# Optimization experiments

Hardware: AMD Instinct MI355X
Metric: run time of the kernel (lower is better)

Reference implementation:

```python
import jax, jax.numpy as jnp
import numpy as np

N_POINTS = 1048576  # batch of evaluation points
HIDDEN = 128
N_HIDDEN_LAYERS = 9  # 128->128 layers between the input and output projections


def setup_inputs() -> dict:
    key = jax.random.key(0)
    ks = jax.random.split(key, 7)
    # Kaiming-ish scale so activations stay O(1) through the deep ReLU stack
    s_in = (2.0 / 4) ** 0.5
    s_h = (2.0 / HIDDEN) ** 0.5
    return {
        "x": jax.random.normal(ks[0], (N_POINTS, 4), dtype=jnp.float32),
        "W0": jax.random.normal(ks[1], (HIDDEN, 4), dtype=jnp.float32) * s_in,
        "b0": jnp.zeros((HIDDEN,), dtype=jnp.float32),
        "Wh": jax.random.normal(ks[2], (N_HIDDEN_LAYERS, HIDDEN, HIDDEN), dtype=jnp.float32) * s_h,
        "bh": jnp.zeros((N_HIDDEN_LAYERS, HIDDEN), dtype=jnp.float32),
        "Wout": jax.random.normal(ks[3], (1, HIDDEN), dtype=jnp.float32) * s_h,
        "bout": jnp.zeros((1,), dtype=jnp.float32),
    }


def reference(x, W0, b0, Wh, bh, Wout, bout):
    # Flatten: x is already [N, 4]; nn.Flatten collapses trailing dims to 4.
    h = jax.nn.relu(jnp.einsum("nd,hd->nh", x, W0) + b0)  # [N, 128]
    # 9 hidden Linear(128,128)+ReLU layers; small fixed layer loop (structural)
    for i in range(N_HIDDEN_LAYERS):
        h = jax.nn.relu(jnp.einsum("nh,oh->no", h, Wh[i]) + bh[i])
    logits = jnp.einsum("nh,oh->no", h, Wout) + bout  # [N, 1], no final ReLU
    return logits
```

## Files before the change

kernel.cpp:

```cpp
#include <hip/hip_runtime.h>
#include <stdint.h>

typedef _Float16 f16x8 __attribute__((ext_vector_type(8)));
typedef __fp16   fp16x2 __attribute__((ext_vector_type(2)));
typedef float    f32x16 __attribute__((ext_vector_type(16)));

union Frag {
  f16x8    v;
  uint32_t w[4];
  _Float16 h[8];
};

union CVec {
  float4 q[4];
  f32x16 v;
};

__device__ __forceinline__ uint32_t pack2h(float a, float b) {
  union { _Float16 h[2]; uint32_t u; } r;
  r.h[0] = (_Float16)a;
  r.h[1] = (_Float16)b;
  return r.u;
}

__device__ __forceinline__ uint32_t pkrtz(float a, float b) {
  union { fp16x2 h2; uint32_t u; } cv;
  cv.h2 = __builtin_amdgcn_cvt_pkrtz(a, b);
  return cv.u;
}

__device__ __forceinline__ void g2lds16(const void* g, void* l) {
  __builtin_amdgcn_global_load_lds(
      (const __attribute__((address_space(1))) uint32_t*)g,
      (__attribute__((address_space(3))) uint32_t*)l, 16, 0, 0);
}

__host__ __device__ __forceinline__ int lam32(int s) {
  return (((s >> 2) ^ (s >> 3)) & 1) ? (s ^ 12) : s;
}

__global__ void prep_kernel(const float* __restrict__ W0, const float* __restrict__ b0,
                            const float* __restrict__ Wh, const float* __restrict__ bh,
                            const float* __restrict__ Wout,
                            _Float16* __restrict__ wfrag, _Float16* __restrict__ w0frag,
                            float* __restrict__ biasC, _Float16* __restrict__ woutf16) {
  const int stride = gridDim.x * blockDim.x;
  for (int idx = blockIdx.x * blockDim.x + threadIdx.x; idx < 154880; idx += stride) {
    if (idx < 147456) {
      const int j = idx & 7, lane = (idx >> 3) & 63, kt = (idx >> 9) & 7,
                ot = (idx >> 12) & 3, l = idx >> 14;
      const int o = ot * 32 + lam32(lane & 31);
      const int k = kt * 16 + (lane >> 5) * 8 + j;
      wfrag[idx] = (_Float16)Wh[(l * 128 + o) * 128 + k];
    } else if (idx < 147456 + 2048) {
      const int i = idx - 147456;
      const int j = i & 7, lane = (i >> 3) & 63, ot = i >> 9;
      const int o = ot * 32 + lam32(lane & 31);
      const int k = (lane >> 5) * 8 + j;
      w0frag[i] = (_Float16)(k < 4 ? W0[o * 4 + k] : 0.0f);
    } else if (idx < 147456 + 2048 + 1280) {
      const int i = idx - (147456 + 2048);
      const int r = i & 15, hh = (i >> 4) & 1, ot = (i >> 5) & 3, l = i >> 7;
      const int slot = (r & 3) + 8 * (r >> 2) + 4 * hh;
      const int o = ot * 32 + lam32(slot);
      biasC[i] = (l == 0) ? b0[o] : bh[(l - 1) * 128 + o];
    } else {
      const int i = idx - (147456 + 2048 + 1280);
      const int j = i & 7, lane = (i >> 3) & 63, kt = i >> 9;
      const int k = kt * 16 + (lane >> 5) * 8 + j;
      woutf16[i] = ((lane & 31) == 0) ? (_Float16)Wout[k] : (_Float16)0.0f;
    }
  }
}

__global__ __launch_bounds__(256, 2) void mlp_fused(
    const float* __restrict__ x,
    const _Float16* __restrict__ wfrag,
    const _Float16* __restrict__ w0frag,
    const float* __restrict__ biasCg,
    const _Float16* __restrict__ woutf16,
    const float* __restrict__ boutp,
    float* __restrict__ out) {
  __shared__ __align__(16) unsigned char ldsW[2][32768];
  __shared__ __align__(16) float ldsBiasC[1280];

  const int t    = threadIdx.x;
  const int lane = t & 63;
  const int wv   = t >> 6;
  const int h    = lane >> 5;
  const int ln   = lane & 31;
  const long rowbase = (long)blockIdx.x * 256 + wv * 64;

  {
    const unsigned char* src = (const unsigned char*)wfrag;
#pragma unroll
    for (int i = 0; i < 8; ++i) {
      const int off = i * 4096 + t * 16;
      g2lds16(src + off, &ldsW[0][off]);
    }
    const unsigned char* bsrc = (const unsigned char*)biasCg;
    g2lds16(bsrc + t * 16, (unsigned char*)ldsBiasC + t * 16);
    if (t < 64) g2lds16(bsrc + (256 + t) * 16, (unsigned char*)ldsBiasC + (256 + t) * 16);
  }

  Frag   B[2][8];
  f32x16 acc[4][2];
  const f32x16 fzero = (f32x16)0.0f;

  auto load_cvec = [&](int l, int ot) -> f32x16 {
    CVec cv;
    const float* p = ldsBiasC + ((l * 4 + ot) * 2 + h) * 16;
#pragma unroll
    for (int g = 0; g < 4; ++g) cv.q[g] = *(const float4*)(p + g * 4);
    return cv.v;
  };

  Frag xb[2];
#pragma unroll
  for (int nt = 0; nt < 2; ++nt) {
    float4 xv = make_float4(0.f, 0.f, 0.f, 0.f);
    if (h == 0) xv = *(const float4*)(x + (rowbase + nt * 32 + ln) * 4);
    xb[nt].w[0] = pack2h(xv.x, xv.y);
    xb[nt].w[1] = pack2h(xv.z, xv.w);
    xb[nt].w[2] = 0u;
    xb[nt].w[3] = 0u;
  }

  __syncthreads();

#pragma unroll
  for (int ot = 0; ot < 4; ++ot) {
    const f16x8 a0 = *(const f16x8*)(w0frag + ot * 512 + lane * 8);
    const f32x16 cvec = load_cvec(0, ot);
    acc[ot][0] = __builtin_amdgcn_mfma_f32_32x32x16_f16(a0, xb[0].v, cvec, 0, 0, 0);
    acc[ot][1] = __builtin_amdgcn_mfma_f32_32x32x16_f16(a0, xb[1].v, cvec, 0, 0, 0);
  }

  auto do_epilogue = [&]() {
#pragma unroll
    for (int ot = 0; ot < 4; ++ot) {
#pragma unroll
      for (int nt = 0; nt < 2; ++nt) {
#pragma unroll
        for (int u = 0; u < 2; ++u) {
          Frag nb;
#pragma unroll
          for (int j = 0; j < 4; ++j) {
            const uint32_t cv = pkrtz(acc[ot][nt][8 * u + 2 * j],
                                      acc[ot][nt][8 * u + 2 * j + 1]);
            uint32_t r;
            asm("v_pk_max_f16 %0, %1, %2" : "=v"(r) : "v"(cv), "v"(0u));
            nb.w[j] = r;
          }
          B[nt][ot * 2 + u] = nb;
        }
      }
    }
  };

#pragma unroll
  for (int l = 1; l <= 9; ++l) {
    if (l < 9) {
      const unsigned char* src = (const unsigned char*)wfrag + (size_t)l * 32768;
#pragma unroll
      for (int i = 0; i < 8; ++i) {
        const int off = i * 4096 + t * 16;
        g2lds16(src + off, &ldsW[l & 1][off]);
      }
    }
    do_epilogue();
    const unsigned char* wl = &ldsW[(l - 1) & 1][0];

    f16x8 a[4];
#pragma unroll
    for (int ot = 0; ot < 4; ++ot)
      a[ot] = *(const f16x8*)(wl + ot * 8192 + lane * 16);

#pragma unroll
    for (int kt = 0; kt < 8; ++kt) {
#pragma unroll
      for (int ot = 0; ot < 4; ++ot) {
        if (kt == 0) {
          const f32x16 cvec = load_cvec(l, ot);
          acc[ot][0] = __builtin_amdgcn_mfma_f32_32x32x16_f16(a[ot], B[0][kt].v, cvec, 0, 0, 0);
          acc[ot][1] = __builtin_amdgcn_mfma_f32_32x32x16_f16(a[ot], B[1][kt].v, cvec, 0, 0, 0);
        } else {
          acc[ot][0] = __builtin_amdgcn_mfma_f32_32x32x16_f16(a[ot], B[0][kt].v, acc[ot][0], 0, 0, 0);
          acc[ot][1] = __builtin_amdgcn_mfma_f32_32x32x16_f16(a[ot], B[1][kt].v, acc[ot][1], 0, 0, 0);
        }
        if (kt < 7)
          a[ot] = *(const f16x8*)(wl + ot * 8192 + (kt + 1) * 1024 + lane * 16);
        __builtin_amdgcn_sched_group_barrier(0x008, 2, 0);
        if (kt < 7)
          __builtin_amdgcn_sched_group_barrier(0x100, 1, 0);
      }
    }
    if (l < 9) __syncthreads();
  }

  {
    Frag wa[8];
#pragma unroll
    for (int kt = 0; kt < 8; ++kt)
      wa[kt].v = *(const f16x8*)(woutf16 + kt * 512 + lane * 8);
    const float boutv = *boutp;

    do_epilogue();

    f32x16 accO0 = fzero, accO1 = fzero;
#pragma unroll
    for (int kt = 0; kt < 8; ++kt) {
      accO0 = __builtin_amdgcn_mfma_f32_32x32x16_f16(wa[kt].v, B[0][kt].v, accO0, 0, 0, 0);
      accO1 = __builtin_amdgcn_mfma_f32_32x32x16_f16(wa[kt].v, B[1][kt].v, accO1, 0, 0, 0);
    }
    if (h == 0) {
      out[rowbase + ln]      = accO0[0] + boutv;
      out[rowbase + 32 + ln] = accO1[0] + boutv;
    }
  }
}

extern "C" void kernel_launch(void* const* d_in, const int* in_sizes, int n_in,
                              void* d_out, int out_size, void* d_ws, size_t ws_size,
                              hipStream_t stream) {
  (void)n_in; (void)out_size; (void)ws_size;
  const float* x    = (const float*)d_in[0];
  const float* W0   = (const float*)d_in[1];
  const float* b0   = (const float*)d_in[2];
  const float* Wh   = (const float*)d_in[3];
  const float* bh   = (const float*)d_in[4];
  const float* Wout = (const float*)d_in[5];
  const float* bout = (const float*)d_in[6];
  float* out = (float*)d_out;

  char* ws = (char*)d_ws;
  _Float16* wfrag   = (_Float16*)(ws);
  _Float16* w0frag  = (_Float16*)(ws + 294912);
  float*    biasC   = (float*)(ws + 299008);
  _Float16* woutf16 = (_Float16*)(ws + 304128);

  const int n = in_sizes[0] / 4;

  prep_kernel<<<dim3(160), dim3(256), 0, stream>>>(W0, b0, Wh, bh, Wout,
                                                   wfrag, w0frag, biasC, woutf16);
  mlp_fused<<<dim3(n / 256), dim3(256), 0, stream>>>(x, wfrag, w0frag, biasC,
                                                     woutf16, bout, out);
}
```

Baseline: 250.6 us.

## Replace block barriers with per-wave LDS flag handshakes for weight staging

Swaps the per-layer __syncthreads for per-wave producer/consumer counters in LDS (stageCnt/readCnt) polled with s_sleep. Each wave now loads its own slice of the next layer's weights only after every wave has finished reading that buffer. Two layers are prefetched up front, and the epilogue is moved after the first weight fragment loads. The aim is to let waves drift apart instead of stalling together at a barrier, at the cost of spin-wait overhead and a fragile memory-ordering protocol.

```diff
diff --git a/kernel.cpp b/kernel.cpp
--- a/kernel.cpp
+++ b/kernel.cpp
@@ -83,6 +83,8 @@
     float* __restrict__ out) {
   __shared__ __align__(16) unsigned char ldsW[2][32768];
   __shared__ __align__(16) float ldsBiasC[1280];
+  __shared__ int stageCnt[4];
+  __shared__ int readCnt[4];
 
   const int t    = threadIdx.x;
   const int lane = t & 63;
@@ -92,15 +94,19 @@
   const long rowbase = (long)blockIdx.x * 256 + wv * 64;
 
   {
-    const unsigned char* src = (const unsigned char*)wfrag;
 #pragma unroll
     for (int i = 0; i < 8; ++i) {
-      const int off = i * 4096 + t * 16;
-      g2lds16(src + off, &ldsW[0][off]);
-    }
-    const unsigned char* bsrc = (const unsigned char*)biasCg;
-    g2lds16(bsrc + t * 16, (unsigned char*)ldsBiasC + t * 16);
-    if (t < 64) g2lds16(bsrc + (256 + t) * 16, (unsigned char*)ldsBiasC + (256 + t) * 16);
+      const int off = (wv * 8 + i) * 1024 + lane * 16;
+      g2lds16((const unsigned char*)wfrag + off, &ldsW[0][off]);
+      g2lds16((const unsigned char*)wfrag + 32768 + off, &ldsW[1][off]);
+    }
+    if (wv == 0) {
+#pragma unroll
+      for (int i = 0; i < 5; ++i)
+        g2lds16((const unsigned char*)biasCg + i * 1024 + lane * 16,
+                (unsigned char*)ldsBiasC + i * 1024 + lane * 16);
+    }
+    if (t < 4) { stageCnt[t] = 2; readCnt[t] = 0; }
   }
 
   Frag   B[2][8];
@@ -126,6 +132,7 @@
     xb[nt].w[3] = 0u;
   }
 
+  asm volatile("s_waitcnt vmcnt(0)" ::: "memory");
   __syncthreads();
 
 #pragma unroll
@@ -158,23 +165,32 @@
     }
   };
 
+  auto spin_ge = [&](volatile int* flag, int target) {
+    while (*flag < target) __builtin_amdgcn_s_sleep(1);
+  };
+
 #pragma unroll
   for (int l = 1; l <= 9; ++l) {
-    if (l < 9) {
-      const unsigned char* src = (const unsigned char*)wfrag + (size_t)l * 32768;
-#pragma unroll
-      for (int i = 0; i < 8; ++i) {
-        const int off = i * 4096 + t * 16;
-        g2lds16(src + off, &ldsW[l & 1][off]);
-      }
-    }
-    do_epilogue();
+    if (l >= 2 && l <= 8) {
+      __builtin_amdgcn_sched_barrier(0);
+      asm volatile("s_waitcnt vmcnt(0)" ::: "memory");
+      *(volatile int*)&stageCnt[wv] = l + 1;
+      __builtin_amdgcn_sched_barrier(0);
+    }
+    if (l >= 3) {
+#pragma unroll
+      for (int w = 0; w < 4; ++w) spin_ge(&stageCnt[w], l);
+      __builtin_amdgcn_sched_barrier(0);
+      asm volatile("" ::: "memory");
+    }
     const unsigned char* wl = &ldsW[(l - 1) & 1][0];
 
     f16x8 a[4];
 #pragma unroll
     for (int ot = 0; ot < 4; ++ot)
       a[ot] = *(const f16x8*)(wl + ot * 8192 + lane * 16);
+
+    do_epilogue();
 
 #pragma unroll
     for (int kt = 0; kt < 8; ++kt) {
@@ -195,7 +211,23 @@
           __builtin_amdgcn_sched_group_barrier(0x100, 1, 0);
       }
     }
-    if (l < 9) __syncthreads();
+
+    if (l <= 7) {
+      __builtin_amdgcn_sched_barrier(0);
+      asm volatile("s_waitcnt lgkmcnt(0)" ::: "memory");
+      *(volatile int*)&readCnt[wv] = l;
+      __builtin_amdgcn_sched_barrier(0);
+#pragma unroll
+      for (int w = 0; w < 4; ++w) spin_ge(&readCnt[w], l);
+      __builtin_amdgcn_sched_barrier(0);
+      const unsigned char* src = (const unsigned char*)wfrag + (size_t)(l + 1) * 32768;
+      unsigned char* dst = &ldsW[(l + 1) & 1][0];
+#pragma unroll
+      for (int i = 0; i < 8; ++i) {
+        const int off = (wv * 8 + i) * 1024 + lane * 16;
+        g2lds16(src + off, dst + off);
+      }
+    }
   }
 
   {
```

After: 290.9 us. 1.16x slower.
